# Kernel optimization log

Hardware: AMD Instinct MI355X
Metric: run time of the kernel (lower is better)

## Reference

```python
import jax, jax.numpy as jnp
import numpy as np

B, CIN, H, W = 2, 3, 768, 768
CB = 32          # backbone out_channels (= channels_mid for heads)
ORDER = 5
MARGIN = 3.0     # ScaledTanh margin of refinement head


def _conv(x, w, b, pad):
    # x: [N,C,H,W], w: [O,I,kh,kw]
    y = jax.lax.conv_general_dilated(x, w, (1, 1), [(pad, pad), (pad, pad)],
                                     dimension_numbers=('NCHW', 'OIHW', 'NCHW'))
    return y + b[None, :, None, None]


def _readout(x, w1, b1, s, t, w2, b2, pad):
    # conv(k) -> batchnorm(eval, folded to scale/shift) -> relu -> dropout(eval=id) -> conv1x1
    h = _conv(x, w1, b1, pad)
    h = jax.nn.relu(h * s[None, :, None, None] + t[None, :, None, None])
    return _conv(h, w2, b2, 0)


def setup_inputs() -> dict:
    key = jax.random.key(0)
    ks = iter(jax.random.split(key, 16))
    def rn(shape, scale=0.05):
        return jax.random.normal(next(ks), shape, jnp.float32) * scale
    d = {'inputs': jax.random.normal(next(ks), (B, CIN, H, W), jnp.float32)}
    d['bb_w'] = rn((CB, CIN, 3, 3)); d['bb_b'] = jnp.zeros((CB,), jnp.float32)
    def head(name, k, cout):
        d[name + '_w1'] = rn((CB, CB, k, k)); d[name + '_b1'] = jnp.zeros((CB,), jnp.float32)
        d[name + '_s'] = jnp.ones((CB,), jnp.float32); d[name + '_t'] = jnp.zeros((CB,), jnp.float32)
        d[name + '_w2'] = rn((cout, CB, 1, 1)); d[name + '_b2'] = jnp.zeros((cout,), jnp.float32)
    head('score', 3, 2)
    head('loc', 7, 2)
    head('four', 7, ORDER * 4)
    head('ref', 7, 2)
    return d


def reference(inputs, bb_w, bb_b,
              score_w1, score_b1, score_s, score_t, score_w2, score_b2,
              loc_w1, loc_b1, loc_s, loc_t, loc_w2, loc_b2,
              four_w1, four_b1, four_s, four_t, four_w2, four_b2,
              ref_w1, ref_b1, ref_s, ref_t, ref_w2, ref_b2):
    # backbone (simple conv + relu; out_channels is an int so contour == refinement features)
    feats = jax.nn.relu(_conv(inputs, bb_w, bb_b, 1))
    scores = _readout(feats, score_w1, score_b1, score_s, score_t, score_w2, score_b2, 1)
    locations = _readout(feats, loc_w1, loc_b1, loc_s, loc_t, loc_w2, loc_b2, 3)
    fourier = _readout(feats, four_w1, four_b1, four_s, four_t, four_w2, four_b2, 3)
    # ReadOut final activation ScaledTanh(3.0), then CPNCore multiplies by internal margin 1.0;
    # feature HW == input HW (stride 1), so F.interpolate is a no-op.
    refinement = jnp.tanh(_readout(feats, ref_w1, ref_b1, ref_s, ref_t, ref_w2, ref_b2, 3)) * MARGIN
    return (scores, locations, refinement, fourier)
```

## Files before the change

### kernel.cpp

```cpp
#include <hip/hip_runtime.h>
#include <hip/hip_bf16.h>
#include <cmath>

#define HH 768
#define WW 768
#define HWSZ (768*768)

typedef __attribute__((ext_vector_type(8))) short bhalf8;
typedef __attribute__((ext_vector_type(4))) float f32x4;
typedef __attribute__((ext_vector_type(16))) float f32x16;

__device__ inline ushort f2bf(float f) {
  __hip_bfloat16 h = __float2bfloat16(f);
  return *reinterpret_cast<ushort*>(&h);
}

__global__ __launch_bounds__(256) void wxform_kernel(
    const float* __restrict__ w1, const float* __restrict__ b1,
    const float* __restrict__ s,  const float* __restrict__ t,
    ushort* __restrict__ wT, float* __restrict__ bb, int npos)
{
  int i = blockIdx.x * 256 + threadIdx.x;
  if (i < npos * 1024) {
    int pos = i >> 10, mc = i & 1023, m = mc >> 5, c = mc & 31;
    wT[i] = f2bf(w1[(m * 32 + c) * npos + pos] * s[m]);
  }
  if (i < 32) bb[i] = b1[i] * s[i] + t[i];
}

__global__ __launch_bounds__(256) void backbone_kernel(
    const float* __restrict__ x, const float* __restrict__ w,
    const float* __restrict__ bias, ushort* __restrict__ feats)
{
  int p = blockIdx.x * 256 + threadIdx.x;
  int bb  = p / HWSZ;
  int rem = p - bb * HWSZ;
  int y   = rem / WW;
  int xx  = rem - y * WW;
  const float* xb = x + (size_t)bb * 3 * HWSZ;

  float v[3][3][3];
  #pragma unroll
  for (int c = 0; c < 3; c++)
    #pragma unroll
    for (int dy = 0; dy < 3; dy++)
      #pragma unroll
      for (int dx = 0; dx < 3; dx++) {
        int yy = y + dy - 1, xq = xx + dx - 1;
        v[c][dy][dx] = (yy >= 0 && yy < HH && xq >= 0 && xq < WW)
                         ? xb[(size_t)c * HWSZ + yy * WW + xq] : 0.f;
      }

  union { ushort u[32]; uint4 q[4]; } pk;
  #pragma unroll
  for (int o = 0; o < 32; o++) {
    float acc = bias[o];
    #pragma unroll
    for (int c = 0; c < 3; c++)
      #pragma unroll
      for (int dy = 0; dy < 3; dy++)
        #pragma unroll
        for (int dx = 0; dx < 3; dx++)
          acc = fmaf(w[((o * 3 + c) * 3 + dy) * 3 + dx], v[c][dy][dx], acc);
    pk.u[o] = f2bf(fmaxf(acc, 0.f));
  }
  uint4* dst = (uint4*)(feats + ((size_t)bb * HWSZ + rem) * 32);
  #pragma unroll
  for (int i = 0; i < 4; i++) dst[i] = pk.q[i];
}

template <int COUT, bool DO_TANH>
__device__ inline void head_epilogue(
    const f32x16 acc[2], const float* __restrict__ bbh,
    const float* __restrict__ w2, const float* __restrict__ b2,
    float* __restrict__ out_base, float* mid,
    int wv, int qr, int qc, int kg, int by, int bx, int bb)
{
  #pragma unroll
  for (int n = 0; n < 2; n++) {
    int pix = (wv * 4 + 2 * n + qr) * 16 + qc;
    #pragma unroll
    for (int rg = 0; rg < 4; rg++) {
      int m0 = 8 * rg + 4 * kg;
      f32x4 v;
      #pragma unroll
      for (int j = 0; j < 4; j++)
        v[j] = fmaxf(acc[n][rg * 4 + j] + bbh[m0 + j], 0.f);
      *(f32x4*)(mid + pix * 36 + m0) = v;
    }
  }
  __syncthreads();

  int t = threadIdx.x;
  float mv[32];
  #pragma unroll
  for (int j2 = 0; j2 < 8; j2++)
    *(f32x4*)(mv + 4 * j2) = *(const f32x4*)(mid + t * 36 + 4 * j2);

  int oy = by * 16 + (t >> 4), ox = bx * 16 + (t & 15);
  size_t opix = (size_t)oy * WW + ox;
  float* ob = out_base + (size_t)bb * COUT * HWSZ;
  #pragma unroll
  for (int oc = 0; oc < COUT; oc++) {
    float a2 = b2[oc];
    #pragma unroll
    for (int m = 0; m < 32; m++) a2 = fmaf(w2[oc * 32 + m], mv[m], a2);
    if (DO_TANH) a2 = tanhf(a2) * 3.0f;
    ob[(size_t)oc * HWSZ + opix] = a2;
  }
  __syncthreads();
}

__global__ __launch_bounds__(256, 2) void heads3_kernel(
    const ushort* __restrict__ feats,
    const ushort* __restrict__ wtL, const ushort* __restrict__ wtF,
    const ushort* __restrict__ wtR,
    const float* __restrict__ bbL, const float* __restrict__ bbF,
    const float* __restrict__ bbR,
    const float* __restrict__ w2L, const float* __restrict__ b2L,
    const float* __restrict__ w2F, const float* __restrict__ b2F,
    const float* __restrict__ w2R, const float* __restrict__ b2R,
    float* __restrict__ outL, float* __restrict__ outF, float* __restrict__ outR)
{
  constexpr int TW = 22, CPAD = 40;
  __shared__ __align__(16) char smem[TW * TW * CPAD * 2];
  ushort* tile = (ushort*)smem;

  int bx = blockIdx.x % 48;
  int by = (blockIdx.x / 48) % 48;
  int bb = blockIdx.x / 2304;
  int x0 = bx * 16 - 3, y0 = by * 16 - 3;
  const ushort* fB = feats + (size_t)bb * HWSZ * 32;

  for (int p = threadIdx.x; p < TW * TW; p += 256) {
    int py = p / TW, pxx = p % TW;
    int yy = y0 + py, xx = x0 + pxx;
    uint4 q0 = {0,0,0,0}, q1 = {0,0,0,0}, q2 = {0,0,0,0}, q3 = {0,0,0,0};
    if (yy >= 0 && yy < HH && xx >= 0 && xx < WW) {
      const uint4* src = (const uint4*)(fB + ((size_t)yy * WW + xx) * 32);
      q0 = src[0]; q1 = src[1]; q2 = src[2]; q3 = src[3];
    }
    uint4* dst = (uint4*)(tile + (size_t)p * CPAD);
    dst[0] = q0; dst[1] = q1; dst[2] = q2; dst[3] = q3;
  }
  __syncthreads();

  int l  = threadIdx.x & 63;
  int wv = threadIdx.x >> 6;
  int q  = l & 31;
  int kg = l >> 5;
  int qr = q >> 4, qc = q & 15;

  const ushort* pb = tile + ((wv * 4 + qr) * TW + qc) * CPAD + kg * 8;
  const int aoff = q * 32 + kg * 8;

  f32x16 accL[2] = {};
  f32x16 accF[2] = {};
  f32x16 accR[2] = {};

  #pragma unroll 1
  for (int ky = 0; ky < 7; ky++) {
    const ushort* pbrow = pb + ky * TW * CPAD;
    const ushort* aL = wtL + ky * 7 * 1024 + aoff;
    const ushort* aF = wtF + ky * 7 * 1024 + aoff;
    const ushort* aR = wtR + ky * 7 * 1024 + aoff;

    #pragma unroll
    for (int kx = 0; kx < 7; kx++) {
      bhalf8 fL[2], fF[2], fR[2];
      #pragma unroll
      for (int kh = 0; kh < 2; kh++) {
        fL[kh] = *(const bhalf8*)(aL + kx * 1024 + kh * 16);
        fF[kh] = *(const bhalf8*)(aF + kx * 1024 + kh * 16);
        fR[kh] = *(const bhalf8*)(aR + kx * 1024 + kh * 16);
      }

      bhalf8 bfr[2][2];
      #pragma unroll
      for (int n = 0; n < 2; n++)
        #pragma unroll
        for (int kh = 0; kh < 2; kh++)
          bfr[n][kh] = *(const bhalf8*)(pbrow + kx * CPAD
                                           + n * 2 * TW * CPAD + kh * 16);

      #pragma unroll
      for (int n = 0; n < 2; n++)
        #pragma unroll
        for (int kh = 0; kh < 2; kh++) {
          accL[n] = __builtin_amdgcn_mfma_f32_32x32x16_bf16(fL[kh], bfr[n][kh], accL[n], 0, 0, 0);
          accF[n] = __builtin_amdgcn_mfma_f32_32x32x16_bf16(fF[kh], bfr[n][kh], accF[n], 0, 0, 0);
          accR[n] = __builtin_amdgcn_mfma_f32_32x32x16_bf16(fR[kh], bfr[n][kh], accR[n], 0, 0, 0);
        }
    }
  }

  __syncthreads();
  float* mid = (float*)smem;

  head_epilogue<2,  false>(accL, bbL, w2L, b2L, outL, mid, wv, qr, qc, kg, by, bx, bb);
  head_epilogue<20, false>(accF, bbF, w2F, b2F, outF, mid, wv, qr, qc, kg, by, bx, bb);
  head_epilogue<2,  true >(accR, bbR, w2R, b2R, outR, mid, wv, qr, qc, kg, by, bx, bb);
}

__global__ __launch_bounds__(256, 4) void score_kernel(
    const ushort* __restrict__ feats,
    const ushort* __restrict__ wtS, const float* __restrict__ bbS,
    const float* __restrict__ w2S, const float* __restrict__ b2S,
    float* __restrict__ outS)
{
  constexpr int TW = 18, CPAD = 40;
  constexpr int SMEM_BYTES = 256 * 36 * 4;
  __shared__ __align__(16) char smem[SMEM_BYTES];
  ushort* tile = (ushort*)smem;

  int bx = blockIdx.x % 48;
  int by = (blockIdx.x / 48) % 48;
  int bb = blockIdx.x / 2304;
  int x0 = bx * 16 - 1, y0 = by * 16 - 1;
  const ushort* fB = feats + (size_t)bb * HWSZ * 32;

  for (int p = threadIdx.x; p < TW * TW; p += 256) {
    int py = p / TW, pxx = p % TW;
    int yy = y0 + py, xx = x0 + pxx;
    uint4 q0 = {0,0,0,0}, q1 = {0,0,0,0}, q2 = {0,0,0,0}, q3 = {0,0,0,0};
    if (yy >= 0 && yy < HH && xx >= 0 && xx < WW) {
      const uint4* src = (const uint4*)(fB + ((size_t)yy * WW + xx) * 32);
      q0 = src[0]; q1 = src[1]; q2 = src[2]; q3 = src[3];
    }
    uint4* dst = (uint4*)(tile + (size_t)p * CPAD);
    dst[0] = q0; dst[1] = q1; dst[2] = q2; dst[3] = q3;
  }
  __syncthreads();

  int l  = threadIdx.x & 63;
  int wv = threadIdx.x >> 6;
  int q  = l & 31;
  int kg = l >> 5;
  int qr = q >> 4, qc = q & 15;

  const ushort* pb = tile + ((wv * 4 + qr) * TW + qc) * CPAD + kg * 8;
  const int aoff = q * 32 + kg * 8;

  f32x16 acc[2] = {};

  #pragma unroll
  for (int ky = 0; ky < 3; ky++) {
    #pragma unroll
    for (int kx = 0; kx < 3; kx++) {
      const int tap = ky * 3 + kx;
      bhalf8 a0[2];
      #pragma unroll
      for (int kh = 0; kh < 2; kh++)
        a0[kh] = *(const bhalf8*)(wtS + tap * 1024 + aoff + kh * 16);
      #pragma unroll
      for (int n = 0; n < 2; n++) {
        #pragma unroll
        for (int kh = 0; kh < 2; kh++) {
          bhalf8 bf = *(const bhalf8*)(pb + (ky * TW + kx) * CPAD
                                          + n * 2 * TW * CPAD + kh * 16);
          acc[n] = __builtin_amdgcn_mfma_f32_32x32x16_bf16(a0[kh], bf, acc[n], 0, 0, 0);
        }
      }
    }
  }

  __syncthreads();
  float* mid = (float*)smem;
  head_epilogue<2, false>(acc, bbS, w2S, b2S, outS, mid, wv, qr, qc, kg, by, bx, bb);
}

extern "C" void kernel_launch(void* const* d_in, const int* in_sizes, int n_in,
                              void* d_out, int out_size, void* d_ws, size_t ws_size,
                              hipStream_t stream) {
  const float* input = (const float*)d_in[0];
  const float* bb_w  = (const float*)d_in[1];
  const float* bb_b  = (const float*)d_in[2];

  ushort* feats = (ushort*)d_ws;
  char* base = (char*)d_ws;
  const size_t FEATS_BYTES = (size_t)2 * HWSZ * 32 * 2;
  const size_t WT_STRIDE   = 49 * 1024 * 2;
  ushort* wT0 = (ushort*)(base + FEATS_BYTES);
  float*  bb0 = (float*)(base + FEATS_BYTES + 4 * WT_STRIDE);
  (void)out_size; (void)ws_size; (void)n_in; (void)in_sizes;

  float* out = (float*)d_out;
  float* outS = out;
  float* outL = out + (size_t)4  * HWSZ;
  float* outR = out + (size_t)8  * HWSZ;
  float* outF = out + (size_t)12 * HWSZ;

  const int npos_h[4] = {9, 49, 49, 49};
  for (int h = 0; h < 4; h++) {
    const float* w1 = (const float*)d_in[3 + h * 6 + 0];
    const float* b1 = (const float*)d_in[3 + h * 6 + 1];
    const float* s  = (const float*)d_in[3 + h * 6 + 2];
    const float* t  = (const float*)d_in[3 + h * 6 + 3];
    ushort* wT = (ushort*)((char*)wT0 + h * WT_STRIDE);
    float*  bbv = bb0 + h * 32;
    int n = npos_h[h] * 1024;
    wxform_kernel<<<(n + 255) / 256, 256, 0, stream>>>(w1, b1, s, t, wT, bbv, npos_h[h]);
  }

  backbone_kernel<<<4608, 256, 0, stream>>>(input, bb_w, bb_b, feats);

  const ushort* wtS = (const ushort*)((char*)wT0 + 0 * WT_STRIDE);
  const ushort* wtL = (const ushort*)((char*)wT0 + 1 * WT_STRIDE);
  const ushort* wtF = (const ushort*)((char*)wT0 + 2 * WT_STRIDE);
  const ushort* wtR = (const ushort*)((char*)wT0 + 3 * WT_STRIDE);

  const int GRID = 2 * 48 * 48;

  heads3_kernel<<<GRID, 256, 0, stream>>>(
      feats, wtL, wtF, wtR,
      bb0 + 32, bb0 + 64, bb0 + 96,
      (const float*)d_in[13], (const float*)d_in[14],
      (const float*)d_in[19], (const float*)d_in[20],
      (const float*)d_in[25], (const float*)d_in[26],
      outL, outF, outR);

  score_kernel<<<GRID, 256, 0, stream>>>(
      feats, wtS, bb0 + 0,
      (const float*)d_in[7], (const float*)d_in[8], outS);
}
```

Before: 469.0 us.

## Stage L/F head weights per kernel row in LDS and relayout feature tile

The heads3 kernel now copies each ky row of the loc and fourier bf16 weights into shared memory in an MFMA-friendly layout before computing, instead of reading them from global memory for every wave. The refinement weights still come from global memory. The feature tile is relaid out channel-group-major per row, with the padding dropped to change the LDS bank access pattern. The four weight-transform launches are merged into one 2D-grid kernel. This adds a sync pair per ky iteration and grows LDS use to about 58KB, which may reduce occupancy below the 2 blocks per CU target.

```diff
diff --git a/kernel.cpp b/kernel.cpp
--- a/kernel.cpp
+++ b/kernel.cpp
@@ -15,17 +15,34 @@
   return *reinterpret_cast<ushort*>(&h);
 }
 
-__global__ __launch_bounds__(256) void wxform_kernel(
-    const float* __restrict__ w1, const float* __restrict__ b1,
-    const float* __restrict__ s,  const float* __restrict__ t,
-    ushort* __restrict__ wT, float* __restrict__ bb, int npos)
-{
+__global__ __launch_bounds__(256) void wxform_all_kernel(
+    const float* __restrict__ w1S, const float* __restrict__ b1S,
+    const float* __restrict__ sS,  const float* __restrict__ tS,
+    const float* __restrict__ w1L, const float* __restrict__ b1L,
+    const float* __restrict__ sL,  const float* __restrict__ tL,
+    const float* __restrict__ w1F, const float* __restrict__ b1F,
+    const float* __restrict__ sF,  const float* __restrict__ tF,
+    const float* __restrict__ w1R, const float* __restrict__ b1R,
+    const float* __restrict__ sR,  const float* __restrict__ tR,
+    ushort* __restrict__ wT0, float* __restrict__ bb0, size_t wt_stride_elems)
+{
+  int h = blockIdx.y;
+  const float *w1, *b1, *s, *t;
+  int npos;
+  if (h == 0)      { w1 = w1S; b1 = b1S; s = sS; t = tS; npos = 9;  }
+  else if (h == 1) { w1 = w1L; b1 = b1L; s = sL; t = tL; npos = 49; }
+  else if (h == 2) { w1 = w1F; b1 = b1F; s = sF; t = tF; npos = 49; }
+  else             { w1 = w1R; b1 = b1R; s = sR; t = tR; npos = 49; }
+
+  ushort* wT = wT0 + (size_t)h * wt_stride_elems;
+  float*  bb = bb0 + h * 32;
+
   int i = blockIdx.x * 256 + threadIdx.x;
   if (i < npos * 1024) {
     int pos = i >> 10, mc = i & 1023, m = mc >> 5, c = mc & 31;
     wT[i] = f2bf(w1[(m * 32 + c) * npos + pos] * s[m]);
   }
-  if (i < 32) bb[i] = b1[i] * s[i] + t[i];
+  if (blockIdx.x == 0 && i < 32) bb[i] = b1[i] * s[i] + t[i];
 }
 
 __global__ __launch_bounds__(256) void backbone_kernel(
@@ -122,9 +139,9 @@
     const float* __restrict__ w2R, const float* __restrict__ b2R,
     float* __restrict__ outL, float* __restrict__ outF, float* __restrict__ outR)
 {
-  constexpr int TW = 22, CPAD = 40;
-  __shared__ __align__(16) char smem[TW * TW * CPAD * 2];
+  __shared__ __align__(16) char smem[30976 + 28672];
   ushort* tile = (ushort*)smem;
+  ushort* wrow = (ushort*)(smem + 30976);
 
   int bx = blockIdx.x % 48;
   int by = (blockIdx.x / 48) % 48;
@@ -132,18 +149,20 @@
   int x0 = bx * 16 - 3, y0 = by * 16 - 3;
   const ushort* fB = feats + (size_t)bb * HWSZ * 32;
 
-  for (int p = threadIdx.x; p < TW * TW; p += 256) {
-    int py = p / TW, pxx = p % TW;
-    int yy = y0 + py, xx = x0 + pxx;
+  for (int p = threadIdx.x; p < 22 * 22; p += 256) {
+    int r = p / 22, cl = p - r * 22;
+    int yy = y0 + r, xx = x0 + cl;
     uint4 q0 = {0,0,0,0}, q1 = {0,0,0,0}, q2 = {0,0,0,0}, q3 = {0,0,0,0};
     if (yy >= 0 && yy < HH && xx >= 0 && xx < WW) {
       const uint4* src = (const uint4*)(fB + ((size_t)yy * WW + xx) * 32);
       q0 = src[0]; q1 = src[1]; q2 = src[2]; q3 = src[3];
     }
-    uint4* dst = (uint4*)(tile + (size_t)p * CPAD);
-    dst[0] = q0; dst[1] = q1; dst[2] = q2; dst[3] = q3;
-  }
-  __syncthreads();
+    ushort* dst = tile + r * 704 + cl * 8;
+    *(uint4*)(dst +   0) = q0;
+    *(uint4*)(dst + 176) = q1;
+    *(uint4*)(dst + 352) = q2;
+    *(uint4*)(dst + 528) = q3;
+  }
 
   int l  = threadIdx.x & 63;
   int wv = threadIdx.x >> 6;
@@ -151,8 +170,9 @@
   int kg = l >> 5;
   int qr = q >> 4, qc = q & 15;
 
-  const ushort* pb = tile + ((wv * 4 + qr) * TW + qc) * CPAD + kg * 8;
-  const int aoff = q * 32 + kg * 8;
+  const ushort* pbB = tile + (wv * 4 + qr) * 704 + kg * 176 + qc * 8;
+  const ushort* aB  = wrow + kg * 256 + q * 8;
+  const ushort* aRb = wtR + q * 32 + kg * 8;
 
   f32x16 accL[2] = {};
   f32x16 accF[2] = {};
@@ -160,28 +180,39 @@
 
   #pragma unroll 1
   for (int ky = 0; ky < 7; ky++) {
-    const ushort* pbrow = pb + ky * TW * CPAD;
-    const ushort* aL = wtL + ky * 7 * 1024 + aoff;
-    const ushort* aF = wtF + ky * 7 * 1024 + aoff;
-    const ushort* aR = wtR + ky * 7 * 1024 + aoff;
+    {
+      const ushort* rowL = wtL + ky * 7168;
+      const ushort* rowF = wtF + ky * 7168;
+      #pragma unroll
+      for (int j = 0; j < 7; j++) {
+        int c = j * 256 + (int)threadIdx.x;
+        int h = (c >= 896) ? 1 : 0;
+        int o = (c - h * 896) * 8;
+        bhalf8 v = *(const bhalf8*)((h ? rowF : rowL) + o);
+        int tap = o >> 10, rem = o & 1023;
+        *(bhalf8*)(wrow + tap * 2048 + h * 1024 + ((rem >> 3) & 3) * 256 + (rem >> 5) * 8) = v;
+      }
+    }
+    __syncthreads();
+
+    const ushort* pbrow = pbB + ky * 704;
+    const ushort* aR = aRb + ky * 7168;
 
     #pragma unroll
     for (int kx = 0; kx < 7; kx++) {
       bhalf8 fL[2], fF[2], fR[2];
       #pragma unroll
       for (int kh = 0; kh < 2; kh++) {
-        fL[kh] = *(const bhalf8*)(aL + kx * 1024 + kh * 16);
-        fF[kh] = *(const bhalf8*)(aF + kx * 1024 + kh * 16);
+        fL[kh] = *(const bhalf8*)(aB + kx * 2048 +        kh * 512);
+        fF[kh] = *(const bhalf8*)(aB + kx * 2048 + 1024 + kh * 512);
         fR[kh] = *(const bhalf8*)(aR + kx * 1024 + kh * 16);
       }
-
       bhalf8 bfr[2][2];
       #pragma unroll
       for (int n = 0; n < 2; n++)
         #pragma unroll
         for (int kh = 0; kh < 2; kh++)
-          bfr[n][kh] = *(const bhalf8*)(pbrow + kx * CPAD
-                                           + n * 2 * TW * CPAD + kh * 16);
+          bfr[n][kh] = *(const bhalf8*)(pbrow + n * 1408 + kh * 352 + kx * 8);
 
       #pragma unroll
       for (int n = 0; n < 2; n++)
@@ -192,9 +223,9 @@
           accR[n] = __builtin_amdgcn_mfma_f32_32x32x16_bf16(fR[kh], bfr[n][kh], accR[n], 0, 0, 0);
         }
     }
-  }
-
-  __syncthreads();
+    __syncthreads();
+  }
+
   float* mid = (float*)smem;
 
   head_epilogue<2,  false>(accL, bbL, w2L, b2L, outL, mid, wv, qr, qc, kg, by, bx, bb);
@@ -279,9 +310,9 @@
   ushort* feats = (ushort*)d_ws;
   char* base = (char*)d_ws;
   const size_t FEATS_BYTES = (size_t)2 * HWSZ * 32 * 2;
-  const size_t WT_STRIDE   = 49 * 1024 * 2;
+  const size_t WT_STRIDE_E = 49 * 1024;
   ushort* wT0 = (ushort*)(base + FEATS_BYTES);
-  float*  bb0 = (float*)(base + FEATS_BYTES + 4 * WT_STRIDE);
+  float*  bb0 = (float*)(base + FEATS_BYTES + 4 * WT_STRIDE_E * 2);
   (void)out_size; (void)ws_size; (void)n_in; (void)in_sizes;
 
   float* out = (float*)d_out;
@@ -290,24 +321,20 @@
   float* outR = out + (size_t)8  * HWSZ;
   float* outF = out + (size_t)12 * HWSZ;
 
-  const int npos_h[4] = {9, 49, 49, 49};
-  for (int h = 0; h < 4; h++) {
-    const float* w1 = (const float*)d_in[3 + h * 6 + 0];
-    const float* b1 = (const float*)d_in[3 + h * 6 + 1];
-    const float* s  = (const float*)d_in[3 + h * 6 + 2];
-    const float* t  = (const float*)d_in[3 + h * 6 + 3];
-    ushort* wT = (ushort*)((char*)wT0 + h * WT_STRIDE);
-    float*  bbv = bb0 + h * 32;
-    int n = npos_h[h] * 1024;
-    wxform_kernel<<<(n + 255) / 256, 256, 0, stream>>>(w1, b1, s, t, wT, bbv, npos_h[h]);
-  }
+  dim3 wxgrid(196, 4);
+  wxform_all_kernel<<<wxgrid, 256, 0, stream>>>(
+      (const float*)d_in[3],  (const float*)d_in[4],  (const float*)d_in[5],  (const float*)d_in[6],
+      (const float*)d_in[9],  (const float*)d_in[10], (const float*)d_in[11], (const float*)d_in[12],
+      (const float*)d_in[15], (const float*)d_in[16], (const float*)d_in[17], (const float*)d_in[18],
+      (const float*)d_in[21], (const float*)d_in[22], (const float*)d_in[23], (const float*)d_in[24],
+      wT0, bb0, WT_STRIDE_E);
 
   backbone_kernel<<<4608, 256, 0, stream>>>(input, bb_w, bb_b, feats);
 
-  const ushort* wtS = (const ushort*)((char*)wT0 + 0 * WT_STRIDE);
-  const ushort* wtL = (const ushort*)((char*)wT0 + 1 * WT_STRIDE);
-  const ushort* wtF = (const ushort*)((char*)wT0 + 2 * WT_STRIDE);
-  const ushort* wtR = (const ushort*)((char*)wT0 + 3 * WT_STRIDE);
+  const ushort* wtS = wT0 + 0 * WT_STRIDE_E;
+  const ushort* wtL = wT0 + 1 * WT_STRIDE_E;
+  const ushort* wtF = wT0 + 2 * WT_STRIDE_E;
+  const ushort* wtR = wT0 + 3 * WT_STRIDE_E;
 
   const int GRID = 2 * 48 * 48;
 
```

Result: faster. 414.9 us (-11.5%).
